# Kernel tuning notes

Hardware: AMD Instinct MI355X
Metric: run time of the kernel (lower is better)

## Reference

```python
import jax, jax.numpy as jnp
import numpy as np

D_MODEL, D_STATE, N_HEADS = 1024, 64, 16


def setup_inputs() -> dict:
    key = jax.random.key(0)
    ks = jax.random.split(key, 4)
    B, T = 4, 4096
    s = 1.0 / np.sqrt(D_MODEL)
    x = jax.random.normal(ks[0], (B, T, D_MODEL), dtype=jnp.float32)
    h_prev = jnp.zeros((B, N_HEADS, D_STATE), dtype=jnp.float32)
    gate_w = jax.random.normal(ks[1], (2 * N_HEADS * D_STATE, D_MODEL), dtype=jnp.float32) * s
    # torch init: forget-gate bias = 1, input-gate bias = 0
    gate_b = jnp.concatenate([jnp.ones(N_HEADS * D_STATE), jnp.zeros(N_HEADS * D_STATE)]).astype(jnp.float32)
    value_w = jax.random.normal(ks[2], (N_HEADS * D_STATE, D_MODEL), dtype=jnp.float32) * s
    out_w = jax.random.normal(ks[3], (D_MODEL, N_HEADS * D_STATE), dtype=jnp.float32) * s
    return {"x": x, "h_prev": h_prev, "gate_w": gate_w, "gate_b": gate_b, "value_w": value_w, "out_w": out_w}


def reference(x, h_prev, gate_w, gate_b, value_w, out_w):
    B, T, _ = x.shape
    H, S = N_HEADS, D_STATE
    gates = (jnp.einsum('btd,gd->btg', x, gate_w) + gate_b).reshape(B, T, 2, H, S)
    A = jax.nn.sigmoid(gates[:, :, 0])   # [B,T,H,S] forget gate
    Bg = jax.nn.sigmoid(gates[:, :, 1])  # [B,T,H,S] input gate
    V = jnp.einsum('btd,vd->btv', x, value_w).reshape(B, T, H, S)

    def step(h, inp):
        a_t, bv_t = inp
        h = a_t * h + bv_t
        return h, h

    # time-major for scan; precompute B*V elementwise product
    a_tm = jnp.moveaxis(A, 1, 0)                # [T,B,H,S]
    bv_tm = jnp.moveaxis(Bg * V, 1, 0)          # [T,B,H,S]
    h_last, h_seq = jax.lax.scan(step, h_prev, (a_tm, bv_tm))
    h_flat = jnp.moveaxis(h_seq, 0, 1).reshape(B, T, H * S)
    y = jnp.einsum('btv,dv->btd', h_flat, out_w)  # dropout is identity at p=0/eval
    return y, h_last
```

## Files before the change

### kernel.cpp

```cpp
#include <hip/hip_runtime.h>
#include <cstdint>
#include <cstddef>


typedef _Float16 f16;
typedef _Float16 f16x2 __attribute__((ext_vector_type(2)));
typedef _Float16 f16x8 __attribute__((ext_vector_type(8)));
typedef float    f32x16 __attribute__((ext_vector_type(16)));

__device__ __forceinline__ void gload_lds16(const void* g, void* l) {
  __builtin_amdgcn_global_load_lds(
      (const __attribute__((address_space(1))) void*)g,
      (__attribute__((address_space(3))) void*)l, 16, 0, 0);
}

__device__ __forceinline__ float sigmoidf_(float x) {
  return 1.0f / (1.0f + __expf(-x));
}

__global__ __launch_bounds__(256) void cast_pack(
    const float* __restrict__ x, const float* __restrict__ gw,
    const float* __restrict__ vw, const float* __restrict__ ow,
    f16* __restrict__ xh, f16* __restrict__ wgv, f16* __restrict__ owb) {
  const int XG = 2097152, GG = 262144, VG = 131072, OG = 131072;
  int id = blockIdx.x * 256 + threadIdx.x;
  const float* src;
  f16* dst;
  if (id < XG) {
    src = x + (size_t)id * 8;
    dst = xh + (size_t)id * 8;
  } else if (id < XG + GG) {
    int g = id - XG;
    int row = g >> 7, col = g & 127;
    int drow = (row < 1024) ? row : (1024 + 2 * (row - 1024));
    src = gw + ((size_t)row << 10) + col * 8;
    dst = wgv + ((size_t)drow << 10) + col * 8;
  } else if (id < XG + GG + VG) {
    int g = id - XG - GG;
    int row = g >> 7, col = g & 127;
    int drow = 1024 + 2 * row + 1;
    src = vw + ((size_t)row << 10) + col * 8;
    dst = wgv + ((size_t)drow << 10) + col * 8;
  } else if (id < XG + GG + VG + OG) {
    int g = id - XG - GG - VG;
    src = ow + (size_t)g * 8;
    dst = owb + (size_t)g * 8;
  } else {
    return;
  }
  float4 v0 = ((const float4*)src)[0], v1 = ((const float4*)src)[1];
  f16x8 o;
  o[0] = (f16)v0.x; o[1] = (f16)v0.y; o[2] = (f16)v0.z; o[3] = (f16)v0.w;
  o[4] = (f16)v1.x; o[5] = (f16)v1.y; o[6] = (f16)v1.z; o[7] = (f16)v1.w;
  *(f16x8*)dst = o;
}

template <int EPI>
__global__ __launch_bounds__(256, 3) void gemm_bt(
    const f16* __restrict__ A, const f16* __restrict__ Bw,
    const float* __restrict__ gate_b,
    void* __restrict__ o0v, void* __restrict__ o1v) {
  constexpr int K = 1024;
  __shared__ __align__(16) f16 S[17920];
  f16* As = S;
  f16* Bs = S + 8192;
  const int tid  = threadIdx.x;
  const int lane = tid & 63;
  const int half = lane >> 5;
  const int l31  = lane & 31;
  const int wv   = tid >> 6;
  const int wrow = wv & 1, wcol = wv >> 1;
  const int n0 = blockIdx.y * 128;
  const int m0 = blockIdx.x * 128;

  const f16* ga[4];
  const f16* gb[4];
  f16* la[4];
  f16* lb[4];
#pragma unroll
  for (int j = 0; j < 4; ++j) {
    int s   = j * 256 + tid;
    int row = s >> 3;
    int kc  = (s & 7) ^ (row & 7);
    ga[j] = A  + (size_t)(n0 + row) * K + kc * 8;
    gb[j] = Bw + (size_t)(m0 + row) * K + kc * 8;
    la[j] = &As[s * 8];
    lb[j] = &Bs[s * 8];
  }

  f32x16 acc[2][2];
#pragma unroll
  for (int mi = 0; mi < 2; ++mi)
#pragma unroll
    for (int ni = 0; ni < 2; ++ni)
#pragma unroll
      for (int e = 0; e < 16; ++e) acc[mi][ni][e] = 0.f;

  for (int k0 = 0; k0 < K; k0 += 64) {
#pragma unroll
    for (int j = 0; j < 4; ++j) gload_lds16(ga[j], la[j]);
#pragma unroll
    for (int j = 0; j < 4; ++j) gload_lds16(gb[j], lb[j]);
#pragma unroll
    for (int j = 0; j < 4; ++j) { ga[j] += 64; gb[j] += 64; }
    __syncthreads();
#pragma unroll
    for (int kk = 0; kk < 4; ++kk) {
      f16x8 af[2], bfv[2];
#pragma unroll
      for (int mi = 0; mi < 2; ++mi) {
        int row  = wrow * 64 + mi * 32 + l31;
        int slot = row * 8 + ((kk * 2 + half) ^ (row & 7));
        af[mi] = *(const f16x8*)(&As[slot * 8]);
      }
#pragma unroll
      for (int ni = 0; ni < 2; ++ni) {
        int row  = wcol * 64 + ni * 32 + l31;
        int slot = row * 8 + ((kk * 2 + half) ^ (row & 7));
        bfv[ni] = *(const f16x8*)(&Bs[slot * 8]);
      }
#pragma unroll
      for (int mi = 0; mi < 2; ++mi)
#pragma unroll
        for (int ni = 0; ni < 2; ++ni)
          acc[mi][ni] = __builtin_amdgcn_mfma_f32_32x32x16_f16(
              af[mi], bfv[ni], acc[mi][ni], 0, 0, 0);
    }
    __syncthreads();
  }

  if (EPI == 1) {
#pragma unroll
    for (int mi = 0; mi < 2; ++mi)
#pragma unroll
      for (int ni = 0; ni < 2; ++ni) {
        const int m = m0 + wcol * 64 + ni * 32 + l31;
#pragma unroll
        for (int r = 0; r < 16; ++r) {
          const int n = n0 + wrow * 64 + mi * 32 + (r & 3) + 8 * (r >> 2) +
                        4 * half;
          ((float*)o0v)[(size_t)n * 1024 + m] = acc[mi][ni][r];
        }
      }
    return;
  }

  if (m0 < 1024) {
#pragma unroll
    for (int mi = 0; mi < 2; ++mi)
#pragma unroll
      for (int ni = 0; ni < 2; ++ni) {
        const int ml = wcol * 64 + ni * 32 + l31;
        const float bias = gate_b[m0 + ml];
#pragma unroll
        for (int r = 0; r < 16; ++r) {
          const int nl = wrow * 64 + mi * 32 + (r & 3) + 8 * (r >> 2) +
                         4 * half;
          S[nl * 136 + ml] = (f16)sigmoidf_(acc[mi][ni][r] + bias);
        }
      }
    __syncthreads();
    f16* o0 = (f16*)o0v;
#pragma unroll
    for (int i = 0; i < 8; ++i) {
      int ch = i * 256 + tid;
      int row = ch >> 4, cc = ch & 15;
      f16x8 vv = *(const f16x8*)&S[row * 136 + cc * 8];
      *(f16x8*)(o0 + (size_t)(n0 + row) * 1024 + m0 + cc * 8) = vv;
    }
  } else {
    const int c0 = (m0 - 1024) >> 1;
#pragma unroll
    for (int mi = 0; mi < 2; ++mi)
#pragma unroll
      for (int ni = 0; ni < 2; ++ni) {
        const int ml = wcol * 64 + ni * 32 + l31;
#pragma unroll
        for (int r = 0; r < 16; ++r) {
          float val = acc[mi][ni][r];
          float pv = __shfl_xor(val, 1, 64);
          if (!(lane & 1)) {
            const int c = ml >> 1;
            const int nl = wrow * 64 + mi * 32 + (r & 3) + 8 * (r >> 2) +
                           4 * half;
            S[nl * 72 + c] =
                (f16)(sigmoidf_(val + gate_b[1024 + c0 + c]) * pv);
          }
        }
      }
    __syncthreads();
    f16* o1 = (f16*)o1v;
#pragma unroll
    for (int i = 0; i < 4; ++i) {
      int ch = i * 256 + tid;
      int row = ch >> 3, cc = ch & 7;
      f16x8 vv = *(const f16x8*)&S[row * 72 + cc * 8];
      *(f16x8*)(o1 + (size_t)(n0 + row) * 1024 + c0 + cc * 8) = vv;
    }
  }
}

__global__ __launch_bounds__(256) void scan_pass1(
    const f16x2* __restrict__ a, const f16x2* __restrict__ bv,
    float2* __restrict__ Ac, float2* __restrict__ Uc) {
  const int c2 = blockIdx.x * 256 + threadIdx.x;
  const int j = blockIdx.y;
  const int b = blockIdx.z;
  const size_t base = ((size_t)(b * 4096 + j * 32)) * 512 + c2;
  float P0 = 1.f, P1 = 1.f, U0 = 0.f, U1 = 0.f;
#pragma unroll 8
  for (int t = 0; t < 32; ++t) {
    const size_t o = base + (size_t)t * 512;
    f16x2 at = a[o], bt = bv[o];
    float a0 = (float)at[0], a1 = (float)at[1];
    P0 *= a0; P1 *= a1;
    U0 = a0 * U0 + (float)bt[0];
    U1 = a1 * U1 + (float)bt[1];
  }
  const size_t o = ((size_t)(b * 128 + j)) * 512 + c2;
  Ac[o] = make_float2(P0, P1);
  Uc[o] = make_float2(U0, U1);
}

__global__ __launch_bounds__(256) void scan_pass2(
    const float* __restrict__ Ac, const float* __restrict__ Uc,
    const float* __restrict__ h_prev, float* __restrict__ Hs,
    float* __restrict__ hlast) {
  __shared__ float SA[4][64], SU[4][64];
  const int tid = threadIdx.x;
  const int seg = tid >> 6;
  const int cl  = tid & 63;
  const int ch  = blockIdx.x * 64 + cl;
  const int b = ch >> 10, c = ch & 1023;
  float A = 1.f, U = 0.f;
  for (int t = 0; t < 32; ++t) {
    const int j = seg * 32 + t;
    const size_t o = ((size_t)(b * 128 + j)) * 1024 + c;
    float av = Ac[o], uv = Uc[o];
    U = av * U + uv;
    A = av * A;
  }
  SA[seg][cl] = A;
  SU[seg][cl] = U;
  __syncthreads();
  float Ae = 1.f, Ue = 0.f;
  for (int s = 0; s < seg; ++s) {
    float av = SA[s][cl], uv = SU[s][cl];
    Ue = av * Ue + uv;
    Ae = av * Ae;
  }
  float H = Ae * h_prev[b * 1024 + c] + Ue;
  for (int t = 0; t < 32; ++t) {
    const int j = seg * 32 + t;
    const size_t o = ((size_t)(b * 128 + j)) * 1024 + c;
    Hs[o] = H;
    H = Ac[o] * H + Uc[o];
  }
  if (seg == 3) hlast[b * 1024 + c] = H;
}

__global__ __launch_bounds__(256) void scan_pass3(
    const f16x2* __restrict__ a, const f16x2* __restrict__ bv,
    const float2* __restrict__ Hs, f16x2* __restrict__ hb) {
  const int c2 = blockIdx.x * 256 + threadIdx.x;
  const int j = blockIdx.y;
  const int b = blockIdx.z;
  const size_t base = ((size_t)(b * 4096 + j * 32)) * 512 + c2;
  float2 H = Hs[((size_t)(b * 128 + j)) * 512 + c2];
  float h0 = H.x, h1 = H.y;
#pragma unroll 8
  for (int t = 0; t < 32; ++t) {
    const size_t o = base + (size_t)t * 512;
    f16x2 at = a[o], bt = bv[o];
    h0 = (float)at[0] * h0 + (float)bt[0];
    h1 = (float)at[1] * h1 + (float)bt[1];
    f16x2 hv; hv[0] = (f16)h0; hv[1] = (f16)h1;
    hb[o] = hv;
  }
}

extern "C" void kernel_launch(void* const* d_in, const int* in_sizes, int n_in,
                              void* d_out, int out_size, void* d_ws,
                              size_t ws_size, hipStream_t stream) {
  const float* x       = (const float*)d_in[0];
  const float* h_prev  = (const float*)d_in[1];
  const float* gate_w  = (const float*)d_in[2];
  const float* gate_b  = (const float*)d_in[3];
  const float* value_w = (const float*)d_in[4];
  const float* out_w   = (const float*)d_in[5];
  float* out = (float*)d_out;

  char* ws = (char*)d_ws;
  f16*   xh   = (f16*)(ws);
  f16*   wgv  = (f16*)(ws + 33554432);
  f16*   owb  = (f16*)(ws + 39845888);
  f16*   abuf = (f16*)(ws + 41943040);
  f16*   bvb  = (f16*)(ws + 75497472);
  float* Ac   = (float*)(ws + 109051904);
  float* Uc   = (float*)(ws + 111149056);
  float* Hs   = (float*)(ws + 113246208);
  float* hlast = out + 16777216;

  cast_pack<<<10240, 256, 0, stream>>>(x, gate_w, value_w, out_w, xh, wgv,
                                       owb);

  gemm_bt<0><<<dim3(24, 128), 256, 0, stream>>>(xh, wgv, gate_b, abuf, bvb);

  scan_pass1<<<dim3(2, 128, 4), 256, 0, stream>>>(
      (const f16x2*)abuf, (const f16x2*)bvb, (float2*)Ac, (float2*)Uc);
  scan_pass2<<<64, 256, 0, stream>>>(Ac, Uc, h_prev, Hs, hlast);
  scan_pass3<<<dim3(2, 128, 4), 256, 0, stream>>>(
      (const f16x2*)abuf, (const f16x2*)bvb, (const float2*)Hs, (f16x2*)xh);

  gemm_bt<1><<<dim3(8, 128), 256, 0, stream>>>(xh, owb, nullptr, out, nullptr);
}
```

Baseline: 365.4 us.

## Replace GEMM with 256x256-tile, double-buffered, 8-wave MFMA kernel

Rewrites both GEMMs as a 512-thread kernel computing 256x256 tiles with 16x16x32 MFMAs, double-buffered LDS staging through direct global-to-LDS loads, and loads for later K-steps issued between compute phases. Block IDs are swizzled so groups of blocks share operand tiles in cache, and s_setprio raises wave priority around the MFMA bursts. The larger tile increases data reuse and hides memory latency better. In exchange it uses 128KB of LDS and many more accumulator registers, which limits occupancy, and the hand-written vmcnt waits must match the issued loads exactly.

```diff
diff --git a/kernel.cpp b/kernel.cpp
--- a/kernel.cpp
+++ b/kernel.cpp
@@ -6,7 +6,7 @@
 typedef _Float16 f16;
 typedef _Float16 f16x2 __attribute__((ext_vector_type(2)));
 typedef _Float16 f16x8 __attribute__((ext_vector_type(8)));
-typedef float    f32x16 __attribute__((ext_vector_type(16)));
+typedef float    f32x4 __attribute__((ext_vector_type(4)));
 
 __device__ __forceinline__ void gload_lds16(const void* g, void* l) {
   __builtin_amdgcn_global_load_lds(
@@ -56,146 +56,221 @@
 }
 
 template <int EPI>
-__global__ __launch_bounds__(256, 3) void gemm_bt(
+__global__ __launch_bounds__(512, 2) void gemm256(
     const f16* __restrict__ A, const f16* __restrict__ Bw,
-    const float* __restrict__ gate_b,
-    void* __restrict__ o0v, void* __restrict__ o1v) {
+    const float* __restrict__ gate_b, void* __restrict__ o0v,
+    void* __restrict__ o1v, int Mtiles) {
   constexpr int K = 1024;
-  __shared__ __align__(16) f16 S[17920];
-  f16* As = S;
-  f16* Bs = S + 8192;
+  __shared__ __align__(16) f16 SH[65536];
+  f16* LA = SH;
+  f16* LB = SH + 32768;
+
   const int tid  = threadIdx.x;
   const int lane = tid & 63;
-  const int half = lane >> 5;
-  const int l31  = lane & 31;
-  const int wv   = tid >> 6;
-  const int wrow = wv & 1, wcol = wv >> 1;
-  const int n0 = blockIdx.y * 128;
-  const int m0 = blockIdx.x * 128;
-
-  const f16* ga[4];
-  const f16* gb[4];
-  f16* la[4];
-  f16* lb[4];
-#pragma unroll
-  for (int j = 0; j < 4; ++j) {
-    int s   = j * 256 + tid;
-    int row = s >> 3;
-    int kc  = (s & 7) ^ (row & 7);
-    ga[j] = A  + (size_t)(n0 + row) * K + kc * 8;
-    gb[j] = Bw + (size_t)(m0 + row) * K + kc * 8;
-    la[j] = &As[s * 8];
-    lb[j] = &Bs[s * 8];
-  }
-
-  f32x16 acc[2][2];
-#pragma unroll
-  for (int mi = 0; mi < 2; ++mi)
-#pragma unroll
-    for (int ni = 0; ni < 2; ++ni)
-#pragma unroll
-      for (int e = 0; e < 16; ++e) acc[mi][ni][e] = 0.f;
-
-  for (int k0 = 0; k0 < K; k0 += 64) {
-#pragma unroll
-    for (int j = 0; j < 4; ++j) gload_lds16(ga[j], la[j]);
-#pragma unroll
-    for (int j = 0; j < 4; ++j) gload_lds16(gb[j], lb[j]);
-#pragma unroll
-    for (int j = 0; j < 4; ++j) { ga[j] += 64; gb[j] += 64; }
-    __syncthreads();
-#pragma unroll
-    for (int kk = 0; kk < 4; ++kk) {
-      f16x8 af[2], bfv[2];
-#pragma unroll
-      for (int mi = 0; mi < 2; ++mi) {
-        int row  = wrow * 64 + mi * 32 + l31;
-        int slot = row * 8 + ((kk * 2 + half) ^ (row & 7));
-        af[mi] = *(const f16x8*)(&As[slot * 8]);
-      }
-#pragma unroll
-      for (int ni = 0; ni < 2; ++ni) {
-        int row  = wcol * 64 + ni * 32 + l31;
-        int slot = row * 8 + ((kk * 2 + half) ^ (row & 7));
-        bfv[ni] = *(const f16x8*)(&Bs[slot * 8]);
-      }
-#pragma unroll
-      for (int mi = 0; mi < 2; ++mi)
-#pragma unroll
-        for (int ni = 0; ni < 2; ++ni)
-          acc[mi][ni] = __builtin_amdgcn_mfma_f32_32x32x16_f16(
-              af[mi], bfv[ni], acc[mi][ni], 0, 0, 0);
+  const int l15  = lane & 15;
+  const int oct4 = lane >> 4;
+  const int wid  = tid >> 6;
+  const int wr   = wid >> 2;
+  const int wc   = wid & 3;
+
+  const int nwg = gridDim.x;
+  const int bid = blockIdx.x;
+  const int swz = (bid & 7) * (nwg >> 3) + (bid >> 3);
+  const int m0 = (swz % Mtiles) * 256;
+  const int n0 = (swz / Mtiles) * 256;
+
+  const int srow = tid >> 2;
+  const int soct = (tid & 3) ^ ((srow >> 1) & 3);
+  const f16* Ag = A  + (size_t)(n0 + srow) * K + soct * 8;
+  const f16* Bg = Bw + (size_t)(m0 + srow) * K + soct * 8;
+  f16* Al = LA + tid * 8;
+  f16* Bl = LB + tid * 8;
+
+  const int fswz  = oct4 ^ ((l15 >> 1) & 3);
+  const int aslot = (wr * 128 + l15) * 4 + fswz;
+  const int bslot = (wc * 64 + l15) * 4 + fswz;
+
+  f32x4 acc[8][4];
+#pragma unroll
+  for (int mm = 0; mm < 8; ++mm)
+#pragma unroll
+    for (int nn = 0; nn < 4; ++nn)
+#pragma unroll
+      for (int e = 0; e < 4; ++e) acc[mm][nn][e] = 0.f;
+
+#define STAGE_A(tl, kh)                                          \
+  do {                                                           \
+    const f16* s_ = Ag + (tl) * 64 + (kh) * 32;                  \
+    f16* d_ = Al + ((tl) & 1) * 16384 + (kh) * 8192;             \
+    gload_lds16(s_, d_);                                         \
+    gload_lds16(s_ + 128 * K, d_ + 4096);                        \
+  } while (0)
+#define STAGE_B(tl, kh)                                          \
+  do {                                                           \
+    const f16* s_ = Bg + (tl) * 64 + (kh) * 32;                  \
+    f16* d_ = Bl + ((tl) & 1) * 16384 + (kh) * 8192;             \
+    gload_lds16(s_, d_);                                         \
+    gload_lds16(s_ + 128 * K, d_ + 4096);                        \
+  } while (0)
+
+  STAGE_A(0, 0); STAGE_B(0, 0);
+  STAGE_A(0, 1); STAGE_B(0, 1);
+  STAGE_A(1, 0); STAGE_B(1, 0);
+  asm volatile("s_waitcnt vmcnt(8)" ::: "memory");
+  __builtin_amdgcn_s_barrier();
+  asm volatile("" ::: "memory");
+
+  f16x8 bf[4];
+  for (int i = 0; i < 8; ++i) {
+    const bool last = (i == 7);
+#pragma unroll
+    for (int ph = 0; ph < 8; ++ph) {
+      const int bb = ph >> 2;
+      const int ks = (ph >> 1) & 1;
+      const int h  = ph & 1;
+
+      f16x8 af[4];
+      if (h == 0) {
+#pragma unroll
+        for (int nn = 0; nn < 4; ++nn)
+          bf[nn] = *(const f16x8*)&LB[bb * 16384 + ks * 8192 +
+                                      (bslot + nn * 64) * 8];
+      }
+#pragma unroll
+      for (int mm = 0; mm < 4; ++mm)
+        af[mm] = *(const f16x8*)&LA[bb * 16384 + ks * 8192 +
+                                    (aslot + (h * 4 + mm) * 64) * 8];
+
+      {
+        constexpr int toff[8] = {1, 1, 2, 2, 2, 2, 3, 3};
+        constexpr int khv[8]  = {1, 1, 0, 0, 1, 1, 0, 0};
+        if (!last || ph < 2) {
+          const int tl = 2 * i + toff[ph];
+          if (ph & 1) STAGE_B(tl, khv[ph]); else STAGE_A(tl, khv[ph]);
+        }
+      }
+
+      __builtin_amdgcn_s_barrier();
+      asm volatile("s_waitcnt lgkmcnt(0)" ::: "memory");
+
+      __builtin_amdgcn_s_setprio(1);
+#pragma unroll
+      for (int mm = 0; mm < 4; ++mm)
+#pragma unroll
+        for (int nn = 0; nn < 4; ++nn)
+          acc[h * 4 + mm][nn] = __builtin_amdgcn_mfma_f32_16x16x32_f16(
+              af[mm], bf[nn], acc[h * 4 + mm][nn], 0, 0, 0);
+      __builtin_amdgcn_s_setprio(0);
+
+      if (ph & 1) {
+        if (!last) {
+          asm volatile("s_waitcnt vmcnt(8)" ::: "memory");
+        } else if (ph == 1) {
+          asm volatile("s_waitcnt vmcnt(8)" ::: "memory");
+        } else if (ph == 3) {
+          asm volatile("s_waitcnt vmcnt(4)" ::: "memory");
+        } else if (ph == 5) {
+          asm volatile("s_waitcnt vmcnt(0)" ::: "memory");
+        }
+      }
+      __builtin_amdgcn_s_barrier();
+      asm volatile("" ::: "memory");
     }
-    __syncthreads();
-  }
+  }
+#undef STAGE_A
+#undef STAGE_B
 
   if (EPI == 1) {
-#pragma unroll
-    for (int mi = 0; mi < 2; ++mi)
-#pragma unroll
-      for (int ni = 0; ni < 2; ++ni) {
-        const int m = m0 + wcol * 64 + ni * 32 + l31;
-#pragma unroll
-        for (int r = 0; r < 16; ++r) {
-          const int n = n0 + wrow * 64 + mi * 32 + (r & 3) + 8 * (r >> 2) +
-                        4 * half;
-          ((float*)o0v)[(size_t)n * 1024 + m] = acc[mi][ni][r];
+    float* out = (float*)o0v;
+#pragma unroll
+    for (int mm = 0; mm < 8; ++mm)
+#pragma unroll
+      for (int nn = 0; nn < 4; ++nn) {
+        const int m = m0 + wc * 64 + nn * 16 + l15;
+#pragma unroll
+        for (int r = 0; r < 4; ++r) {
+          const int n = n0 + wr * 128 + mm * 16 + oct4 * 4 + r;
+          out[(size_t)n * 1024 + m] = acc[mm][nn][r];
         }
       }
     return;
   }
 
   if (m0 < 1024) {
-#pragma unroll
-    for (int mi = 0; mi < 2; ++mi)
-#pragma unroll
-      for (int ni = 0; ni < 2; ++ni) {
-        const int ml = wcol * 64 + ni * 32 + l31;
-        const float bias = gate_b[m0 + ml];
-#pragma unroll
-        for (int r = 0; r < 16; ++r) {
-          const int nl = wrow * 64 + mi * 32 + (r & 3) + 8 * (r >> 2) +
-                         4 * half;
-          S[nl * 136 + ml] = (f16)sigmoidf_(acc[mi][ni][r] + bias);
-        }
-      }
-    __syncthreads();
+    float bias[4];
+#pragma unroll
+    for (int nn = 0; nn < 4; ++nn)
+      bias[nn] = gate_b[m0 + wc * 64 + nn * 16 + l15];
     f16* o0 = (f16*)o0v;
 #pragma unroll
-    for (int i = 0; i < 8; ++i) {
-      int ch = i * 256 + tid;
-      int row = ch >> 4, cc = ch & 15;
-      f16x8 vv = *(const f16x8*)&S[row * 136 + cc * 8];
-      *(f16x8*)(o0 + (size_t)(n0 + row) * 1024 + m0 + cc * 8) = vv;
+    for (int ck = 0; ck < 2; ++ck) {
+      __builtin_amdgcn_s_barrier();
+      asm volatile("" ::: "memory");
+      if (wr == ck) {
+#pragma unroll
+        for (int mm = 0; mm < 8; ++mm)
+#pragma unroll
+          for (int nn = 0; nn < 4; ++nn) {
+            const int ch = wc * 64 + nn * 16 + l15;
+#pragma unroll
+            for (int r = 0; r < 4; ++r) {
+              const int nl = mm * 16 + oct4 * 4 + r;
+              SH[nl * 264 + ch] = (f16)sigmoidf_(acc[mm][nn][r] + bias[nn]);
+            }
+          }
+      }
+      __builtin_amdgcn_s_barrier();
+      asm volatile("" ::: "memory");
+#pragma unroll
+      for (int j = 0; j < 8; ++j) {
+        int s = j * 512 + tid;
+        int row = s >> 5, sl = s & 31;
+        f16x8 vv = *(const f16x8*)&SH[row * 264 + sl * 8];
+        *(f16x8*)(o0 + (size_t)(n0 + ck * 128 + row) * 1024 + m0 + sl * 8) =
+            vv;
+      }
     }
   } else {
     const int c0 = (m0 - 1024) >> 1;
-#pragma unroll
-    for (int mi = 0; mi < 2; ++mi)
-#pragma unroll
-      for (int ni = 0; ni < 2; ++ni) {
-        const int ml = wcol * 64 + ni * 32 + l31;
-#pragma unroll
-        for (int r = 0; r < 16; ++r) {
-          float val = acc[mi][ni][r];
-          float pv = __shfl_xor(val, 1, 64);
-          if (!(lane & 1)) {
-            const int c = ml >> 1;
-            const int nl = wrow * 64 + mi * 32 + (r & 3) + 8 * (r >> 2) +
-                           4 * half;
-            S[nl * 72 + c] =
-                (f16)(sigmoidf_(val + gate_b[1024 + c0 + c]) * pv);
+    float biasv[4];
+#pragma unroll
+    for (int nn = 0; nn < 4; ++nn) {
+      const int ml = wc * 64 + nn * 16 + l15;
+      biasv[nn] = gate_b[1024 + c0 + (ml >> 1)];
+    }
+    f16* o1 = (f16*)o1v;
+#pragma unroll
+    for (int ck = 0; ck < 2; ++ck) {
+      __builtin_amdgcn_s_barrier();
+      asm volatile("" ::: "memory");
+      if (wr == ck) {
+#pragma unroll
+        for (int mm = 0; mm < 8; ++mm)
+#pragma unroll
+          for (int nn = 0; nn < 4; ++nn) {
+            const int ml = wc * 64 + nn * 16 + l15;
+#pragma unroll
+            for (int r = 0; r < 4; ++r) {
+              float val = acc[mm][nn][r];
+              float pv = __shfl_xor(val, 1, 64);
+              if (!(lane & 1)) {
+                const int nl = mm * 16 + oct4 * 4 + r;
+                SH[nl * 136 + (ml >> 1)] =
+                    (f16)(sigmoidf_(val + biasv[nn]) * pv);
+              }
+            }
           }
-        }
-      }
-    __syncthreads();
-    f16* o1 = (f16*)o1v;
-#pragma unroll
-    for (int i = 0; i < 4; ++i) {
-      int ch = i * 256 + tid;
-      int row = ch >> 3, cc = ch & 7;
-      f16x8 vv = *(const f16x8*)&S[row * 72 + cc * 8];
-      *(f16x8*)(o1 + (size_t)(n0 + row) * 1024 + c0 + cc * 8) = vv;
+      }
+      __builtin_amdgcn_s_barrier();
+      asm volatile("" ::: "memory");
+#pragma unroll
+      for (int j = 0; j < 4; ++j) {
+        int s = j * 512 + tid;
+        int row = s >> 4, sl = s & 15;
+        f16x8 vv = *(const f16x8*)&SH[row * 136 + sl * 8];
+        *(f16x8*)(o1 + (size_t)(n0 + ck * 128 + row) * 1024 + c0 + sl * 8) =
+            vv;
+      }
     }
   }
 }
@@ -304,7 +379,7 @@
   cast_pack<<<10240, 256, 0, stream>>>(x, gate_w, value_w, out_w, xh, wgv,
                                        owb);
 
-  gemm_bt<0><<<dim3(24, 128), 256, 0, stream>>>(xh, wgv, gate_b, abuf, bvb);
+  gemm256<0><<<dim3(768), 512, 0, stream>>>(xh, wgv, gate_b, abuf, bvb, 12);
 
   scan_pass1<<<dim3(2, 128, 4), 256, 0, stream>>>(
       (const f16x2*)abuf, (const f16x2*)bvb, (float2*)Ac, (float2*)Uc);
@@ -312,5 +387,5 @@
   scan_pass3<<<dim3(2, 128, 4), 256, 0, stream>>>(
       (const f16x2*)abuf, (const f16x2*)bvb, (const float2*)Hs, (f16x2*)xh);
 
-  gemm_bt<1><<<dim3(8, 128), 256, 0, stream>>>(xh, owb, nullptr, out, nullptr);
-}
+  gemm256<1><<<dim3(256), 512, 0, stream>>>(xh, owb, nullptr, out, nullptr, 4);
+}
```

After: 377.8 us. +3.4%, slower.
